# Optimization experiments

Hardware: AMD Instinct MI355X
Metric: run time of the kernel (lower is better)

Reference implementation:

```python
import jax, jax.numpy as jnp
import numpy as np

B, CIN, COUT, H, W = 8, 128, 128, 64, 64

# kernel-grid base offsets (dy, dx), row-major k = kh*3 + kw, matching torch base_offset-1
BASE = jnp.array([[-1, -1], [-1, 0], [-1, 1],
                  [0, -1], [0, 0], [0, 1],
                  [1, -1], [1, 0], [1, 1]], dtype=jnp.float32)  # [9,2]
CORNER = jnp.array([1, 0, 1, 0, 0, 0, 1, 0, 1], dtype=jnp.float32)  # mask1 per kernel tap
EDGE = jnp.array([0, 1, 0, 1, 0, 1, 0, 1, 0], dtype=jnp.float32)    # mask2 per kernel tap


def conv3x3(x, w, b=None):
    out = jax.lax.conv_general_dilated(
        x, w, window_strides=(1, 1), padding=((1, 1), (1, 1)),
        dimension_numbers=('NCHW', 'OIHW', 'NCHW'))
    if b is not None:
        out = out + b[None, :, None, None]
    return out


def bilinear_sample(x, py, px):
    Bv, C, Hin, Win = x.shape
    y0 = jnp.floor(py)
    x0 = jnp.floor(px)
    wy = py - y0
    wx = px - x0
    y0i = y0.astype(jnp.int32)
    x0i = x0.astype(jnp.int32)
    xf = x.reshape(Bv, C, Hin * Win)

    def corner(yi, xi):
        valid = ((yi >= 0) & (yi < Hin) & (xi >= 0) & (xi < Win)).astype(x.dtype)
        idx = jnp.clip(yi, 0, Hin - 1) * Win + jnp.clip(xi, 0, Win - 1)  # [B,K,Ho,Wo]
        g = jax.vmap(lambda xb, ib: xb[:, ib])(xf, idx)  # [B,C,K,Ho,Wo]
        return g * valid[:, None]

    v00 = corner(y0i, x0i)
    v01 = corner(y0i, x0i + 1)
    v10 = corner(y0i + 1, x0i)
    v11 = corner(y0i + 1, x0i + 1)
    wy = wy[:, None]
    wx = wx[:, None]
    return (v00 * (1 - wy) * (1 - wx) + v01 * (1 - wy) * wx
            + v10 * wy * (1 - wx) + v11 * wy * wx)


def setup_inputs() -> dict:
    key = jax.random.key(0)
    k1, k2, k3 = jax.random.split(key, 3)
    x = jax.random.normal(k1, (B, CIN, H, W), dtype=jnp.float32)
    # small offset-conv weights keep predicted offsets in a realistic sub-pixel range
    w_off = jax.random.normal(k2, (5, CIN, 3, 3), dtype=jnp.float32) * 0.02
    b_off = jnp.zeros((5,), dtype=jnp.float32)
    w = jax.random.normal(k3, (COUT, CIN, 3, 3), dtype=jnp.float32) * (1.0 / np.sqrt(CIN * 9))
    b = jnp.zeros((COUT,), dtype=jnp.float32)
    return {"x": x, "w_off": w_off, "b_off": b_off, "w": w, "b": b}


def reference(x, w_off, b_off, w, b):
    off = conv3x3(x, w_off, b_off)          # [B,5,H,W]
    scale1 = jax.nn.relu(off[:, 2:3]) + 1.0  # corner scale [B,1,H,W]
    scale2 = jax.nn.relu(off[:, 3:4]) + 1.0  # edge scale   [B,1,H,W]
    shift = off[:, :2]                       # equivariant shift vector [B,2,H,W]

    # per-tap scale; center tap gets 0 but its base offset is (0,0) anyway
    scale_k = CORNER[None, :, None, None] * scale1 + EDGE[None, :, None, None] * scale2  # [B,9,H,W]
    # deform offset = scaled_base - base + shift = base*(scale-1) + shift
    delta = BASE[None, :, :, None, None] * (scale_k - 1.0)[:, :, None] + shift[:, None]  # [B,9,2,H,W]

    hs = jnp.arange(H, dtype=x.dtype)
    ws = jnp.arange(W, dtype=x.dtype)
    # sampling positions: p0 + base_k + offset_k (stride=1, pad=1)
    py = hs[None, None, :, None] + BASE[None, :, 0, None, None] + delta[:, :, 0]  # [B,9,H,W]
    px = ws[None, None, None, :] + BASE[None, :, 1, None, None] + delta[:, :, 1]

    sampled = bilinear_sample(x, py, px)  # [B,CIN,9,H,W]
    out = jnp.einsum('bckhw,ock->bohw', sampled, w.reshape(COUT, CIN, 9))
    return out + b[None, :, None, None]
```

## Files before the change

kernel.cpp:

```cpp
#include <hip/hip_runtime.h>

#define Wd 64
#define Hd 64
#define HWp 4096
#define CIN_ 128
#define COUT_ 128

typedef _Float16 f16;
typedef _Float16 h2    __attribute__((ext_vector_type(2)));
typedef _Float16 f16x8 __attribute__((ext_vector_type(8)));
typedef float f32x4    __attribute__((ext_vector_type(4)));

__device__ inline ushort f2h(float f) {
    f16 h = (f16)f;
    return __builtin_bit_cast(ushort, h);
}
__device__ inline h2 gb(const int4& g, int d) {
    return __builtin_bit_cast(h2, (&g.x)[d]);
}
__device__ inline h2 dup(float f) {
    f16 h = (f16)f;
    h2 r; r[0] = h; r[1] = h;
    return r;
}
struct H8 { h2 r[4]; };

__global__ __launch_bounds__(256) void prep_offsets_kernel(
    const float* __restrict__ x, const float* __restrict__ w,
    const float* __restrict__ w_off, const float* __restrict__ b_off,
    ushort* __restrict__ xt, ushort* __restrict__ w_t2,
    int4* __restrict__ midx, float4* __restrict__ mw)
{
    __shared__ char smem[34816];
    int blk = blockIdx.x;
    int t = threadIdx.x;

    if (blk < 256) {
        ushort* tile = (ushort*)smem;
        int b = blk >> 5, yx0 = (blk & 31) << 7;
        const float* xb = x + (size_t)b * CIN_ * HWp + yx0;
        int lanelo = t & 31, grp = t >> 5;
        #pragma unroll
        for (int i = 0; i < 4; i++) {
            int cbase = i * 32 + grp * 4;
            float4 v0 = *(const float4*)(xb + (size_t)(cbase + 0) * HWp + lanelo * 4);
            float4 v1 = *(const float4*)(xb + (size_t)(cbase + 1) * HWp + lanelo * 4);
            float4 v2 = *(const float4*)(xb + (size_t)(cbase + 2) * HWp + lanelo * 4);
            float4 v3 = *(const float4*)(xb + (size_t)(cbase + 3) * HWp + lanelo * 4);
            ushort4 u;
            u.x = f2h(v0.x); u.y = f2h(v1.x); u.z = f2h(v2.x); u.w = f2h(v3.x);
            *(ushort4*)&tile[(lanelo * 4 + 0) * 136 + cbase] = u;
            u.x = f2h(v0.y); u.y = f2h(v1.y); u.z = f2h(v2.y); u.w = f2h(v3.y);
            *(ushort4*)&tile[(lanelo * 4 + 1) * 136 + cbase] = u;
            u.x = f2h(v0.z); u.y = f2h(v1.z); u.z = f2h(v2.z); u.w = f2h(v3.z);
            *(ushort4*)&tile[(lanelo * 4 + 2) * 136 + cbase] = u;
            u.x = f2h(v0.w); u.y = f2h(v1.w); u.z = f2h(v2.w); u.w = f2h(v3.w);
            *(ushort4*)&tile[(lanelo * 4 + 3) * 136 + cbase] = u;
        }
        __syncthreads();
        ushort* dst = xt + ((size_t)b * HWp + yx0) * CIN_;
        int c8 = (t & 15) * 8, yxg = t >> 4;
        #pragma unroll
        for (int i = 0; i < 8; i++) {
            int yxl = i * 16 + yxg;
            int4 v = *(int4*)&tile[yxl * 136 + c8];
            *(int4*)(dst + (size_t)yxl * CIN_ + c8) = v;
        }
    } else if (blk < 832) {
        int i = (blk - 256) * 256 + t;
        int j    = i & 7;
        int lane = (i >> 3) & 63;
        int ii   = (i >> 9) & 3;
        int wm   = (i >> 11) & 1;
        int s    = i >> 12;
        int o = wm * 64 + ii * 16 + (lane & 15);
        int c = (s & 3) * 32 + (lane >> 4) * 8 + j;
        int k = s >> 2;
        w_t2[i] = f2h(w[o * 1152 + c * 9 + k]);
    } else {
        float* wl   = (float*)smem;
        float* part = (float*)(smem + 18432);
        float* der  = (float*)(smem + 22528);
        int blk2 = blk - 832;
        int b = blk2 >> 6;
        int h = blk2 & 63;

        for (int i = t; i < 4608; i += 256) {
            int j = i / 1152;
            int r = i - j * 1152;
            wl[r * 4 + j] = w_off[i];
        }
        __syncthreads();

        int pi = t & 63, cc = t >> 6;
        const float* xb = x + (size_t)(b * CIN_ + cc * 32) * HWp;

        int idx9[9];
        float msk9[9];
        #pragma unroll
        for (int dy = 0; dy < 3; dy++) {
            int hy = h + dy - 1;
            int hyc = min(max(hy, 0), Hd - 1);
            bool vr = (hy >= 0) && (hy < Hd);
            #pragma unroll
            for (int dx = 0; dx < 3; dx++) {
                int wx = pi + dx - 1;
                int wxc = min(max(wx, 0), Wd - 1);
                bool v = vr && (wx >= 0) && (wx < Wd);
                idx9[dy * 3 + dx] = hyc * Wd + wxc;
                msk9[dy * 3 + dx] = v ? 1.0f : 0.0f;
            }
        }

        float o0 = 0.f, o1 = 0.f, o2 = 0.f, o3 = 0.f;
        #pragma unroll 2
        for (int c = 0; c < 32; c++) {
            const float* xp = xb + c * HWp;
            const float* wc = &wl[(cc * 32 + c) * 36];
            float xv[9];
            #pragma unroll
            for (int tp = 0; tp < 9; tp++) xv[tp] = xp[idx9[tp]] * msk9[tp];
            #pragma unroll
            for (int tp = 0; tp < 9; tp++) {
                float4 wj = *(const float4*)&wc[tp * 4];
                o0 += xv[tp] * wj.x; o1 += xv[tp] * wj.y;
                o2 += xv[tp] * wj.z; o3 += xv[tp] * wj.w;
            }
        }
        part[t * 4 + 0] = o0;
        part[t * 4 + 1] = o1;
        part[t * 4 + 2] = o2;
        part[t * 4 + 3] = o3;
        __syncthreads();

        if (t < 64) {
            float s0 = b_off[0], s1 = b_off[1], s2 = b_off[2], s3 = b_off[3];
            #pragma unroll
            for (int q = 0; q < 4; q++) {
                s0 += part[(q * 64 + t) * 4 + 0];
                s1 += part[(q * 64 + t) * 4 + 1];
                s2 += part[(q * 64 + t) * 4 + 2];
                s3 += part[(q * 64 + t) * 4 + 3];
            }
            der[t * 4 + 0] = s0;
            der[t * 4 + 1] = s1;
            der[t * 4 + 2] = fmaxf(s2, 0.f) + 1.f;
            der[t * 4 + 3] = fmaxf(s3, 0.f) + 1.f;
        }
        __syncthreads();

        #pragma unroll
        for (int s = 0; s < 3; s++) {
            int q = t + s * 256;
            if (q < 576) {
                int k = q >> 6;
                int pp = q & 63;
                float sy = der[pp * 4 + 0], sx = der[pp * 4 + 1];
                float sc1 = der[pp * 4 + 2], sc2 = der[pp * 4 + 3];
                int ky = k / 3, kx = k - ky * 3;
                float by = (float)(ky - 1), bx = (float)(kx - 1);
                bool corner = (ky != 1) && (kx != 1);
                bool edge = (ky != 1) ^ (kx != 1);
                float sk = corner ? sc1 : (edge ? sc2 : 0.0f);
                float py = (float)h + by * sk + sy;
                float px = (float)pp + bx * sk + sx;
                float y0f = floorf(py), x0f = floorf(px);
                float wy = py - y0f, wx = px - x0f;
                int y0 = (int)y0f, x0 = (int)x0f;
                int y1 = y0 + 1, x1 = x0 + 1;
                float vy0 = (y0 >= 0 && y0 < Hd) ? 1.f : 0.f;
                float vy1 = (y1 >= 0 && y1 < Hd) ? 1.f : 0.f;
                float vx0 = (x0 >= 0 && x0 < Wd) ? 1.f : 0.f;
                float vx1 = (x1 >= 0 && x1 < Wd) ? 1.f : 0.f;
                int cy0 = min(max(y0, 0), Hd - 1), cy1 = min(max(y1, 0), Hd - 1);
                int cx0 = min(max(x0, 0), Wd - 1), cx1 = min(max(x1, 0), Wd - 1);
                int4 ii;
                ii.x = cy0 * Wd + cx0;
                ii.y = cy0 * Wd + cx1;
                ii.z = cy1 * Wd + cx0;
                ii.w = cy1 * Wd + cx1;
                float4 ww;
                ww.x = (1.f - wy) * (1.f - wx) * vy0 * vx0;
                ww.y = (1.f - wy) * wx * vy0 * vx1;
                ww.z = wy * (1.f - wx) * vy1 * vx0;
                ww.w = wy * wx * vy1 * vx1;
                int addr = (b * 9 + k) * HWp + h * Wd + pp;
                midx[addr] = ii;
                mw[addr] = ww;
            }
        }
    }
}

__global__ __launch_bounds__(512, 1) void deform_gemm_mfma(
    const ushort* __restrict__ xt, const ushort* __restrict__ w_t2,
    const float* __restrict__ bias, const int4* __restrict__ midx,
    const float4* __restrict__ mw, float* __restrict__ out)
{
    __shared__ ushort A_lds[2][2][4096];
    __shared__ ushort S_lds[2][2][128 * 40];

    int t = threadIdx.x;
    int b = blockIdx.x >> 5;
    int rp = blockIdx.x & 31;
    int p0 = rp << 7;
    const ushort* xtb = xt + (size_t)b * HWp * CIN_;

    int p  = t >> 2;
    int c8 = (t & 3) << 3;

    int wv = t >> 6, lane = t & 63;
    int wm = wv & 1, ns = wv >> 1;
    int lm = lane & 15, lq = lane >> 4;

    f32x4 acc[4][2] = {};

    const ushort* cbp[4];
    h2 cwp[4];
    auto loadmeta = [&](int k) {
        int addr = (b * 9 + k) * HWp + p0 + p;
        int4 mi = midx[addr];
        float4 v = mw[addr];
        cbp[0] = xtb + mi.x * CIN_ + c8;
        cbp[1] = xtb + mi.y * CIN_ + c8;
        cbp[2] = xtb + mi.z * CIN_ + c8;
        cbp[3] = xtb + mi.w * CIN_ + c8;
        cwp[0] = dup(v.x); cwp[1] = dup(v.y);
        cwp[2] = dup(v.z); cwp[3] = dup(v.w);
    };

    auto stageA = [&](int buf, int st) {
        const ushort* src = w_t2 + (size_t)st * 8192;
        #pragma unroll
        for (int cc = 0; cc < 2; cc++) {
            const ushort* g = src + cc * 4096 + wv * 512 + lane * 8;
            ushort* l = &A_lds[buf][cc][wv * 512];
            __builtin_amdgcn_global_load_lds(
                (const __attribute__((address_space(1))) unsigned int*)g,
                (__attribute__((address_space(3))) unsigned int*)l, 16, 0, 0);
        }
    };

    int4 Gc[2][4], Gn[2][4];
    auto issue = [&](int st, int4 G[2][4]) {
        #pragma unroll
        for (int cc = 0; cc < 2; cc++) {
            int q = (2 * st + cc) & 3;
            #pragma unroll
            for (int r = 0; r < 4; r++)
                G[cc][r] = *(const int4*)(cbp[r] + q * 32);
        }
    };
    auto commitS = [&](int buf, const int4 G[2][4]) {
        #pragma unroll
        for (int cc = 0; cc < 2; cc++) {
            H8 tmp;
            #pragma unroll
            for (int d = 0; d < 4; d++) {
                h2 r = gb(G[cc][0], d) * cwp[0];
                r = gb(G[cc][1], d) * cwp[1] + r;
                r = gb(G[cc][2], d) * cwp[2] + r;
                r = gb(G[cc][3], d) * cwp[3] + r;
                tmp.r[d] = r;
            }
            *(int4*)&S_lds[buf][cc][p * 40 + c8] = __builtin_bit_cast(int4, tmp);
        }
    };

    loadmeta(0);
    issue(0, Gc);
    stageA(0, 0);
    commitS(0, Gc);
    __syncthreads();

    for (int st = 0; st < 18; st++) {
        int cur = st & 1, nb = cur ^ 1;
        bool prod = (st + 1 < 18);
        if (prod) {
            if (((st + 1) & 1) == 0) loadmeta((st + 1) >> 1);
            issue(st + 1, Gn);
            stageA(nb, st + 1);
        }

        #pragma unroll
        for (int cc = 0; cc < 2; cc++) {
            f16x8 af[4], bfr[2];
            #pragma unroll
            for (int i = 0; i < 4; i++)
                af[i] = *(const f16x8*)&A_lds[cur][cc][(wm * 4 + i) * 512 + lane * 8];
            #pragma unroll
            for (int f = 0; f < 2; f++)
                bfr[f] = *(const f16x8*)&S_lds[cur][cc][(ns * 32 + f * 16 + lm) * 40 + lq * 8];
            #pragma unroll
            for (int i = 0; i < 4; i++)
                #pragma unroll
                for (int f = 0; f < 2; f++)
                    acc[i][f] = __builtin_amdgcn_mfma_f32_16x16x32_f16(
                        af[i], bfr[f], acc[i][f], 0, 0, 0);
        }

        if (prod) {
            commitS(nb, Gn);
            #pragma unroll
            for (int cc = 0; cc < 2; cc++)
                #pragma unroll
                for (int r = 0; r < 4; r++) Gc[cc][r] = Gn[cc][r];
        }
        __syncthreads();
    }

    #pragma unroll
    for (int i = 0; i < 4; i++) {
        #pragma unroll
        for (int r = 0; r < 4; r++) {
            int o = wm * 64 + i * 16 + lq * 4 + r;
            float bv = bias[o];
            float* orow = out + (size_t)(b * COUT_ + o) * HWp + p0 + ns * 32 + lm;
            #pragma unroll
            for (int f = 0; f < 2; f++)
                orow[f * 16] = acc[i][f][r] + bv;
        }
    }
}

extern "C" void kernel_launch(void* const* d_in, const int* in_sizes, int n_in,
                              void* d_out, int out_size, void* d_ws, size_t ws_size,
                              hipStream_t stream) {
    const float* x     = (const float*)d_in[0];
    const float* w_off = (const float*)d_in[1];
    const float* b_off = (const float*)d_in[2];
    const float* w     = (const float*)d_in[3];
    const float* bias  = (const float*)d_in[4];
    float* out = (float*)d_out;

    char* ws = (char*)d_ws;
    ushort* xt   = (ushort*)ws;
    ushort* w_t2 = (ushort*)(ws + 8388608);
    int4*   midx = (int4*)(ws + 8683520);
    float4* mwp  = (float4*)(ws + 13402112);

    prep_offsets_kernel<<<1344, 256, 0, stream>>>(x, w, w_off, b_off,
                                                  xt, w_t2, midx, mwp);
    deform_gemm_mfma<<<256, 512, 0, stream>>>(xt, w_t2, bias, midx, mwp, out);
}
```

Measured before the change: 122.9 us.

## Compute bilinear metadata in GEMM kernel and deepen gather pipeline to two stages

The prep kernel now writes only the per-pixel offset/scale vector, and the GEMM kernel recomputes the bilinear indices and weights per tap. This drops the large int4/float4 metadata arrays and the global traffic to write and read them. The main loop is also restructured into a manually unrolled three-deep schedule: gathers are issued two stages ahead, with explicit waitcnt and s_barrier calls. The cost is more ALU work and register pressure in the GEMM kernel, and the hand-placed waitcnt counts must stay correct.

After: 116.1 us. 5.6% less time.

```diff
diff --git a/kernel.cpp b/kernel.cpp
--- a/kernel.cpp
+++ b/kernel.cpp
@@ -29,7 +29,7 @@
     const float* __restrict__ x, const float* __restrict__ w,
     const float* __restrict__ w_off, const float* __restrict__ b_off,
     ushort* __restrict__ xt, ushort* __restrict__ w_t2,
-    int4* __restrict__ midx, float4* __restrict__ mw)
+    float4* __restrict__ der)
 {
     __shared__ char smem[34816];
     int blk = blockIdx.x;
@@ -80,7 +80,6 @@
     } else {
         float* wl   = (float*)smem;
         float* part = (float*)(smem + 18432);
-        float* der  = (float*)(smem + 22528);
         int blk2 = blk - 832;
         int b = blk2 >> 6;
         int h = blk2 & 63;
@@ -142,60 +141,20 @@
                 s2 += part[(q * 64 + t) * 4 + 2];
                 s3 += part[(q * 64 + t) * 4 + 3];
             }
-            der[t * 4 + 0] = s0;
-            der[t * 4 + 1] = s1;
-            der[t * 4 + 2] = fmaxf(s2, 0.f) + 1.f;
-            der[t * 4 + 3] = fmaxf(s3, 0.f) + 1.f;
-        }
-        __syncthreads();
-
-        #pragma unroll
-        for (int s = 0; s < 3; s++) {
-            int q = t + s * 256;
-            if (q < 576) {
-                int k = q >> 6;
-                int pp = q & 63;
-                float sy = der[pp * 4 + 0], sx = der[pp * 4 + 1];
-                float sc1 = der[pp * 4 + 2], sc2 = der[pp * 4 + 3];
-                int ky = k / 3, kx = k - ky * 3;
-                float by = (float)(ky - 1), bx = (float)(kx - 1);
-                bool corner = (ky != 1) && (kx != 1);
-                bool edge = (ky != 1) ^ (kx != 1);
-                float sk = corner ? sc1 : (edge ? sc2 : 0.0f);
-                float py = (float)h + by * sk + sy;
-                float px = (float)pp + bx * sk + sx;
-                float y0f = floorf(py), x0f = floorf(px);
-                float wy = py - y0f, wx = px - x0f;
-                int y0 = (int)y0f, x0 = (int)x0f;
-                int y1 = y0 + 1, x1 = x0 + 1;
-                float vy0 = (y0 >= 0 && y0 < Hd) ? 1.f : 0.f;
-                float vy1 = (y1 >= 0 && y1 < Hd) ? 1.f : 0.f;
-                float vx0 = (x0 >= 0 && x0 < Wd) ? 1.f : 0.f;
-                float vx1 = (x1 >= 0 && x1 < Wd) ? 1.f : 0.f;
-                int cy0 = min(max(y0, 0), Hd - 1), cy1 = min(max(y1, 0), Hd - 1);
-                int cx0 = min(max(x0, 0), Wd - 1), cx1 = min(max(x1, 0), Wd - 1);
-                int4 ii;
-                ii.x = cy0 * Wd + cx0;
-                ii.y = cy0 * Wd + cx1;
-                ii.z = cy1 * Wd + cx0;
-                ii.w = cy1 * Wd + cx1;
-                float4 ww;
-                ww.x = (1.f - wy) * (1.f - wx) * vy0 * vx0;
-                ww.y = (1.f - wy) * wx * vy0 * vx1;
-                ww.z = wy * (1.f - wx) * vy1 * vx0;
-                ww.w = wy * wx * vy1 * vx1;
-                int addr = (b * 9 + k) * HWp + h * Wd + pp;
-                midx[addr] = ii;
-                mw[addr] = ww;
-            }
+            float4 d;
+            d.x = s0;
+            d.y = s1;
+            d.z = fmaxf(s2, 0.f) + 1.f;
+            d.w = fmaxf(s3, 0.f) + 1.f;
+            der[(size_t)b * HWp + h * Wd + t] = d;
         }
     }
 }
 
 __global__ __launch_bounds__(512, 1) void deform_gemm_mfma(
     const ushort* __restrict__ xt, const ushort* __restrict__ w_t2,
-    const float* __restrict__ bias, const int4* __restrict__ midx,
-    const float4* __restrict__ mw, float* __restrict__ out)
+    const float* __restrict__ bias, const float4* __restrict__ der,
+    float* __restrict__ out)
 {
     __shared__ ushort A_lds[2][2][4096];
     __shared__ ushort S_lds[2][2][128 * 40];
@@ -215,18 +174,39 @@
 
     f32x4 acc[4][2] = {};
 
+    int pg = p0 + p;
+    float fh = (float)(pg >> 6), fp = (float)(pg & 63);
+    float4 dv = der[(size_t)b * HWp + pg];
+
     const ushort* cbp[4];
-    h2 cwp[4];
-    auto loadmeta = [&](int k) {
-        int addr = (b * 9 + k) * HWp + p0 + p;
-        int4 mi = midx[addr];
-        float4 v = mw[addr];
-        cbp[0] = xtb + mi.x * CIN_ + c8;
-        cbp[1] = xtb + mi.y * CIN_ + c8;
-        cbp[2] = xtb + mi.z * CIN_ + c8;
-        cbp[3] = xtb + mi.w * CIN_ + c8;
-        cwp[0] = dup(v.x); cwp[1] = dup(v.y);
-        cwp[2] = dup(v.z); cwp[3] = dup(v.w);
+
+    auto computeMeta = [&](int k, h2 (&cw)[4]) {
+        int ky = (k * 11) >> 5;
+        int kx = k - ky * 3;
+        float by = (float)(ky - 1), bx = (float)(kx - 1);
+        bool corner = (ky != 1) && (kx != 1);
+        bool edge = (ky != 1) ^ (kx != 1);
+        float sk = corner ? dv.z : (edge ? dv.w : 0.0f);
+        float py = fh + by * sk + dv.x;
+        float px = fp + bx * sk + dv.y;
+        float y0f = floorf(py), x0f = floorf(px);
+        float wy = py - y0f, wx = px - x0f;
+        int y0 = (int)y0f, x0 = (int)x0f;
+        int y1 = y0 + 1, x1 = x0 + 1;
+        float vy0 = (y0 >= 0 && y0 < Hd) ? 1.f : 0.f;
+        float vy1 = (y1 >= 0 && y1 < Hd) ? 1.f : 0.f;
+        float vx0 = (x0 >= 0 && x0 < Wd) ? 1.f : 0.f;
+        float vx1 = (x1 >= 0 && x1 < Wd) ? 1.f : 0.f;
+        int cy0 = min(max(y0, 0), Hd - 1), cy1 = min(max(y1, 0), Hd - 1);
+        int cx0 = min(max(x0, 0), Wd - 1), cx1 = min(max(x1, 0), Wd - 1);
+        cbp[0] = xtb + (cy0 * Wd + cx0) * CIN_ + c8;
+        cbp[1] = xtb + (cy0 * Wd + cx1) * CIN_ + c8;
+        cbp[2] = xtb + (cy1 * Wd + cx0) * CIN_ + c8;
+        cbp[3] = xtb + (cy1 * Wd + cx1) * CIN_ + c8;
+        cw[0] = dup((1.f - wy) * (1.f - wx) * vy0 * vx0);
+        cw[1] = dup((1.f - wy) * wx * vy0 * vx1);
+        cw[2] = dup(wy * (1.f - wx) * vy1 * vx0);
+        cw[3] = dup(wy * wx * vy1 * vx1);
     };
 
     auto stageA = [&](int buf, int st) {
@@ -241,8 +221,7 @@
         }
     };
 
-    int4 Gc[2][4], Gn[2][4];
-    auto issue = [&](int st, int4 G[2][4]) {
+    auto issue = [&](int st, int4 (&G)[2][4]) {
         #pragma unroll
         for (int cc = 0; cc < 2; cc++) {
             int q = (2 * st + cc) & 3;
@@ -251,37 +230,22 @@
                 G[cc][r] = *(const int4*)(cbp[r] + q * 32);
         }
     };
-    auto commitS = [&](int buf, const int4 G[2][4]) {
+    auto commitS = [&](int buf, const int4 (&G)[2][4], const h2 (&cw)[4]) {
         #pragma unroll
         for (int cc = 0; cc < 2; cc++) {
             H8 tmp;
             #pragma unroll
             for (int d = 0; d < 4; d++) {
-                h2 r = gb(G[cc][0], d) * cwp[0];
-                r = gb(G[cc][1], d) * cwp[1] + r;
-                r = gb(G[cc][2], d) * cwp[2] + r;
-                r = gb(G[cc][3], d) * cwp[3] + r;
+                h2 r = gb(G[cc][0], d) * cw[0];
+                r = gb(G[cc][1], d) * cw[1] + r;
+                r = gb(G[cc][2], d) * cw[2] + r;
+                r = gb(G[cc][3], d) * cw[3] + r;
                 tmp.r[d] = r;
             }
             *(int4*)&S_lds[buf][cc][p * 40 + c8] = __builtin_bit_cast(int4, tmp);
         }
     };
-
-    loadmeta(0);
-    issue(0, Gc);
-    stageA(0, 0);
-    commitS(0, Gc);
-    __syncthreads();
-
-    for (int st = 0; st < 18; st++) {
-        int cur = st & 1, nb = cur ^ 1;
-        bool prod = (st + 1 < 18);
-        if (prod) {
-            if (((st + 1) & 1) == 0) loadmeta((st + 1) >> 1);
-            issue(st + 1, Gn);
-            stageA(nb, st + 1);
-        }
-
+    auto mfmaSec = [&](int cur) {
         #pragma unroll
         for (int cc = 0; cc < 2; cc++) {
             f16x8 af[4], bfr[2];
@@ -298,16 +262,51 @@
                     acc[i][f] = __builtin_amdgcn_mfma_f32_16x16x32_f16(
                         af[i], bfr[f], acc[i][f], 0, 0, 0);
         }
-
-        if (prod) {
-            commitS(nb, Gn);
-            #pragma unroll
-            for (int cc = 0; cc < 2; cc++)
-                #pragma unroll
-                for (int r = 0; r < 4; r++) Gc[cc][r] = Gn[cc][r];
-        }
-        __syncthreads();
+    };
+
+    int4 GA[2][4], GB[2][4];
+    h2 cwA[4], cwB[4];
+
+    computeMeta(0, cwA);
+    stageA(0, 0);
+    __builtin_amdgcn_sched_barrier(0);
+    issue(0, GA);
+    commitS(0, GA, cwA);
+    issue(1, GB);
+    asm volatile("s_waitcnt vmcnt(8) lgkmcnt(0)" ::: "memory");
+    __builtin_amdgcn_s_barrier();
+    __builtin_amdgcn_sched_barrier(0);
+
+#define BODY(ST, GC, GI, CWC, DOMETA, CWI)                                   \
+    {                                                                        \
+        int cur_ = (ST) & 1, nb_ = cur_ ^ 1;                                 \
+        if ((ST) + 1 < 18) stageA(nb_, (ST) + 1);                            \
+        __builtin_amdgcn_sched_barrier(0);                                   \
+        if ((ST) + 2 < 18) {                                                 \
+            if (DOMETA) computeMeta(((ST) + 2) >> 1, CWI);                   \
+            issue((ST) + 2, GI);                                             \
+        }                                                                    \
+        mfmaSec(cur_);                                                       \
+        if ((ST) + 1 < 18) commitS(nb_, GC, CWC);                            \
+        if ((ST) + 2 < 18) {                                                 \
+            asm volatile("s_waitcnt vmcnt(8) lgkmcnt(0)" ::: "memory");      \
+        } else {                                                             \
+            asm volatile("s_waitcnt vmcnt(0) lgkmcnt(0)" ::: "memory");      \
+        }                                                                    \
+        __builtin_amdgcn_s_barrier();                                        \
+        __builtin_amdgcn_sched_barrier(0);                                   \
     }
+
+    for (int su = 0; su < 4; su++) {
+        int st = su << 2;
+        BODY(st,     GB, GA, cwA, 1, cwB);
+        BODY(st + 1, GA, GB, cwB, 0, cwB);
+        BODY(st + 2, GB, GA, cwB, 1, cwA);
+        BODY(st + 3, GA, GB, cwA, 0, cwA);
+    }
+    BODY(16, GB, GA, cwA, 0, cwA);
+    BODY(17, GA, GB, cwA, 0, cwA);
+#undef BODY
 
     #pragma unroll
     for (int i = 0; i < 4; i++) {
@@ -336,10 +335,9 @@
     char* ws = (char*)d_ws;
     ushort* xt   = (ushort*)ws;
     ushort* w_t2 = (ushort*)(ws + 8388608);
-    int4*   midx = (int4*)(ws + 8683520);
-    float4* mwp  = (float4*)(ws + 13402112);
+    float4* der  = (float4*)(ws + 8683520);
 
     prep_offsets_kernel<<<1344, 256, 0, stream>>>(x, w, w_off, b_off,
-                                                  xt, w_t2, midx, mwp);
-    deform_gemm_mfma<<<256, 512, 0, stream>>>(xt, w_t2, bias, midx, mwp, out);
-}
+                                                  xt, w_t2, der);
+    deform_gemm_mfma<<<256, 512, 0, stream>>>(xt, w_t2, bias, der, out);
+}
```
